# Performance work log

Hardware: AMD Instinct MI355X
Metric: run time of the kernel (lower is better)

## Reference

```python
import jax, jax.numpy as jnp
import numpy as np

K = 9                # snake kernel size
CENTER = K // 2
EXT = 1.0            # extend_scope
EPS = 1e-5           # GroupNorm eps (torch default)


def conv2d(x, w, b, stride, padding):
    out = jax.lax.conv_general_dilated(
        x, w, window_strides=stride, padding=padding,
        dimension_numbers=("NCHW", "OIHW", "NCHW"))
    return out + b[None, :, None, None]


def group_norm(x, gamma, beta, groups):
    B, C, H, W = x.shape
    xg = x.reshape(B, groups, C // groups, H, W)
    mu = xg.mean(axis=(2, 3, 4), keepdims=True)
    var = xg.var(axis=(2, 3, 4), keepdims=True)
    xn = ((xg - mu) / jnp.sqrt(var + EPS)).reshape(B, C, H, W)
    return xn * gamma[None, :, None, None] + beta[None, :, None, None]


def setup_inputs() -> dict:
    key = jax.random.key(0)
    ks = jax.random.split(key, 6)
    B, Cin, Cout, H, W = 4, 64, 64, 128, 128
    x = jax.random.normal(ks[0], (B, Cin, H, W), jnp.float32)
    w_off = jax.random.normal(ks[1], (2 * K, Cin, 3, 3), jnp.float32) * 0.05
    b_off = jax.random.normal(ks[2], (2 * K,), jnp.float32) * 0.01
    g_gn_off = jnp.ones((2 * K,), jnp.float32)
    b_gn_off = jnp.zeros((2 * K,), jnp.float32)
    w_dsc = jax.random.normal(ks[3], (Cout, Cin, K, 1), jnp.float32) * 0.05
    b_dsc = jax.random.normal(ks[4], (Cout,), jnp.float32) * 0.01
    g_gn = jnp.ones((Cout,), jnp.float32)
    b_gn = jnp.zeros((Cout,), jnp.float32)
    return {"x": x, "w_off": w_off, "b_off": b_off,
            "g_gn_off": g_gn_off, "b_gn_off": b_gn_off,
            "w_dsc": w_dsc, "b_dsc": b_dsc, "g_gn": g_gn, "b_gn": b_gn}


def reference(x, w_off, b_off, g_gn_off, b_gn_off, w_dsc, b_dsc, g_gn, b_gn):
    B, Cin, H, W = x.shape
    # offset branch: conv3x3 -> GN(K groups over 2K chans) -> tanh
    off = conv2d(x, w_off, b_off, (1, 1), "SAME")
    off = jnp.tanh(group_norm(off, g_gn_off, b_gn_off, K))
    y_off = off[:, :K]                              # morph=0 uses y offsets, [B,K,H,W]

    # cumulative offsets outward from the kernel center (center entry = 0)
    upper = jnp.cumsum(y_off[:, CENTER + 1:], axis=1)
    lower = jnp.flip(jnp.cumsum(jnp.flip(y_off[:, :CENTER], axis=1), axis=1), axis=1)
    y_off_new = jnp.concatenate(
        [lower, jnp.zeros_like(y_off[:, :1]), upper], axis=1)   # [B,K,H,W]

    # coordinate maps (pixel space)
    y_coord = jnp.arange(H, dtype=x.dtype)[None, None, :, None] + EXT * y_off_new
    x_spread = jnp.linspace(-CENTER, CENTER, K).astype(x.dtype)
    x_coord = jnp.broadcast_to(
        jnp.arange(W, dtype=x.dtype)[None, None, None, :]
        + x_spread[None, :, None, None], y_coord.shape)
    # rearrange b k h w -> b (h k) w
    y_map = y_coord.transpose(0, 2, 1, 3).reshape(B, H * K, W)
    x_map = x_coord.transpose(0, 2, 1, 3).reshape(B, H * K, W)

    # bilinear grid_sample, align_corners=True; clamp-to-range == torch's
    # _coordinate_map_scaling(clamp + [-1,1] normalize) then grid_sample
    yc = jnp.clip(y_map, 0.0, H - 1.0)
    xc = jnp.clip(x_map, 0.0, W - 1.0)
    y0 = jnp.floor(yc); x0 = jnp.floor(xc)
    wy = yc - y0; wx = xc - x0
    y0i = y0.astype(jnp.int32); x0i = x0.astype(jnp.int32)
    y1i = jnp.minimum(y0i + 1, H - 1); x1i = jnp.minimum(x0i + 1, W - 1)

    def samp(f, y0i, y1i, x0i, x1i, wy, wx):
        # f: [C,H,W]; indices/weights: [K*H, W] -> [C, K*H, W]
        v00 = f[:, y0i, x0i]; v01 = f[:, y0i, x1i]
        v10 = f[:, y1i, x0i]; v11 = f[:, y1i, x1i]
        return (v00 * (1 - wy) * (1 - wx) + v01 * (1 - wy) * wx
                + v10 * wy * (1 - wx) + v11 * wy * wx)

    deformed = jax.vmap(samp)(x, y0i, y1i, x0i, x1i, wy, wx)  # [B,C,K*H,W]

    # snake conv: kernel (K,1), stride (K,1), then GN(out//4) + ReLU
    out = conv2d(deformed, w_dsc, b_dsc, (K, 1), "VALID")      # [B,Cout,H,W]
    out = group_norm(out, g_gn, b_gn, w_dsc.shape[0] // 4)
    return jax.nn.relu(out)
```

## Files before the change

kernel.cpp:

```cpp
#include <hip/hip_runtime.h>
#include <hip/hip_bf16.h>
#include <math.h>

#define B 4
#define C 64
#define H 128
#define W 128
#define KK 9
#define CENTER 4
#define HW (H*W)
#define HP 130
#define WP 130

typedef __attribute__((ext_vector_type(8))) short short8;
typedef __attribute__((ext_vector_type(4))) float f4;

#define OFF_OFFT   0
#define OFF_XB     786432
#define OFF_WB     2949632
#define OFF_WOB    2968064
#define OFF_CSUM   2972672
#define OFF_OSUM   2980864

__device__ __forceinline__ unsigned bf16pack(float a, float b) {
    unsigned ua = __builtin_bit_cast(unsigned, a) + 0x8000u;
    unsigned ub = __builtin_bit_cast(unsigned, b) + 0x8000u;
    return __builtin_amdgcn_perm(ub, ua, 0x07060302);
}

__device__ __forceinline__ unsigned lerp_pack(unsigned a, unsigned b, float fw) {
    float alo = __builtin_bit_cast(float, a << 16);
    float ahi = __builtin_bit_cast(float, a & 0xffff0000u);
    float blo = __builtin_bit_cast(float, b << 16);
    float bhi = __builtin_bit_cast(float, b & 0xffff0000u);
    float slo = alo + fw * (blo - alo);
    float shi = ahi + fw * (bhi - ahi);
    return bf16pack(slo, shi);
}

__device__ __forceinline__ float fast_tanh(float x) {
    float e = __expf(2.f * x);
    return 1.f - 2.f * __builtin_amdgcn_rcpf(e + 1.f);
}

__global__ __launch_bounds__(256) void k_prep(const float* __restrict__ x,
                                              const float* __restrict__ w_dsc,
                                              const float* __restrict__ w_off,
                                              unsigned short* __restrict__ xb,
                                              unsigned short* __restrict__ wb,
                                              unsigned short* __restrict__ wob,
                                              float* __restrict__ csum) {
    int bid = blockIdx.x;
    int tid = threadIdx.x;
    if (bid < 2048) {
        __shared__ float lt[64 * 33];
        int xcd = bid & 7, i = bid >> 3;
        int c = i & 3, hc = (i >> 2) & 15, b = i >> 6;
        int h = (xcd << 4) | hc;
        int w0 = c * 32;
        int ciA = tid >> 2, gA = tid & 3;
        int wlB = tid >> 3, cgB = tid & 7;

        if (c == 0 && tid < 8)
            *(uint4*)(xb + ((size_t)(b * HP + h + 1) * WP) * 64 + tid * 8)
                = make_uint4(0, 0, 0, 0);
        if (c == 3 && tid < 8)
            *(uint4*)(xb + (((size_t)(b * HP + h + 1) * WP) + WP - 1) * 64 + tid * 8)
                = make_uint4(0, 0, 0, 0);
        {
            const float* src = x + ((size_t)(b * C + ciA) * HW) + h * W + w0 + gA * 8;
            float4 v0 = *(const float4*)src;
            float4 v1 = *(const float4*)(src + 4);
            float* d = lt + ciA * 33 + gA * 8;
            d[0] = v0.x; d[1] = v0.y; d[2] = v0.z; d[3] = v0.w;
            d[4] = v1.x; d[5] = v1.y; d[6] = v1.z; d[7] = v1.w;
        }
        __syncthreads();
        {
            unsigned u[4];
#pragma unroll
            for (int i2 = 0; i2 < 4; i2++) {
                float lo = lt[(cgB * 8 + 2 * i2)     * 33 + wlB];
                float hi = lt[(cgB * 8 + 2 * i2 + 1) * 33 + wlB];
                u[i2] = bf16pack(lo, hi);
            }
            *(uint4*)(xb + ((size_t)((b * HP + h + 1) * WP + w0 + wlB + 1)) * 64 + cgB * 8) =
                make_uint4(u[0], u[1], u[2], u[3]);
        }
    } else if (bid < 2048 + 8) {
        int r = bid - 2048;
        int b = r >> 1, which = r & 1;
        unsigned short* dst = xb + ((size_t)(b * HP + which * (HP - 1)) * WP) * 64;
        for (int t = tid; t < WP * 64 / 8; t += 256)
            *(uint4*)(dst + t * 8) = make_uint4(0, 0, 0, 0);
    } else if (bid < 2048 + 8 + 180) {
        int idx = (bid - (2048 + 8)) * 256 + tid;
        if (idx < KK * C * C) {
            int k  = idx >> 12;
            int r  = idx & 4095;
            int co = r >> 6;
            int ci = r & 63;
            unsigned u = __builtin_bit_cast(unsigned, w_dsc[(co * C + ci) * KK + k]);
            u = (u + 0x7fffu + ((u >> 16) & 1u)) >> 16;
            wb[idx] = (unsigned short)u;
        } else if (idx < KK * C * C + 9 * 16 * 64) {
            int r   = idx - KK * C * C;
            int tap = r >> 10;
            int j   = (r >> 6) & 15;
            int ci  = r & 63;
            float v = (j < 10) ? w_off[(j * C + ci) * 9 + tap] : 0.f;
            unsigned u = __builtin_bit_cast(unsigned, v);
            u = (u + 0x7fffu + ((u >> 16) & 1u)) >> 16;
            wob[r] = (unsigned short)u;
        }
    } else {
        int z = bid - (2048 + 8 + 180);
        int base = z * 1024 + tid * 4;
        *(f4*)(csum + base) = 0;
    }
}

__global__ __launch_bounds__(256, 4) void k_offconv(const unsigned short* __restrict__ xb,
                                                    const unsigned short* __restrict__ wob,
                                                    const float* __restrict__ b_off,
                                                    float* __restrict__ offT,
                                                    float* __restrict__ osum16) {
    __shared__ unsigned short wlds[1152 * 8];
    __shared__ float red[80];
    int bid = blockIdx.x;
    int xcd  = bid & 7;
    int i    = bid >> 3;
    int b    = i >> 5;
    int rest = i & 31;
    int h    = (xcd << 4) | (rest >> 1);
    int half = rest & 1;
    int tid  = threadIdx.x;
    int wid  = tid >> 6;
    int lane = tid & 63;
    int lm = lane & 15, qd = lane >> 4;
    int pw = half * 64 + wid * 16;

    for (int c = tid; c < 1152; c += 256) {
        int row = c >> 3, g = c & 7;
        uint4 v = *(const uint4*)(wob + c * 8);
        int dst = (g ^ (row & 7)) * 144 + row;
        *(uint4*)(wlds + dst * 8) = v;
    }
    __syncthreads();

    f4 acc = 0;
    const unsigned short* xrow = xb + ((size_t)(b * HP + h) * WP) * 64;
#pragma unroll
    for (int s = 0; s < 2; s++) {
        int co_ofs = s * 32 + qd * 8;
        short8 a_[9];
#pragma unroll
        for (int t = 0; t < 9; t++) {
            int ky = t / 3, kx = t - 3 * (t / 3);
            a_[t] = *(const short8*)(xrow +
                ((size_t)(ky * WP + pw + lm + kx)) * 64 + co_ofs);
        }
#pragma unroll
        for (int t = 0; t < 9; t++) {
            int row = t * 16 + lm;
            int chunk = (((s * 4 + qd) ^ (lm & 7)) * 144) + row;
            short8 w = *(const short8*)(wlds + chunk * 8);
            acc = __builtin_amdgcn_mfma_f32_16x16x32_bf16(a_[t], w, acc, 0, 0, 0);
        }
    }

    float bo = b_off[lm];
    float sv = 0.f, sq = 0.f;
    int pixbase = (b * H + h) * W;
#pragma unroll
    for (int r = 0; r < 4; r++) {
        float val = acc[r] + bo;
        int p = pw + qd * 4 + r;
        if (lm < 10) {
            offT[(size_t)(pixbase + p) * 12 + lm] = val;
            sv += val; sq += val * val;
        }
    }
    sv += __shfl_xor(sv, 16); sv += __shfl_xor(sv, 32);
    sq += __shfl_xor(sq, 16); sq += __shfl_xor(sq, 32);
    if (lane < 16 && lm < 10) {
        red[(wid * 10 + lm) * 2]     = sv;
        red[(wid * 10 + lm) * 2 + 1] = sq;
    }
    __syncthreads();
    if (tid < 20) {
        int j = tid >> 1, comp = tid & 1;
        float s = red[j * 2 + comp] + red[(10 + j) * 2 + comp] +
                  red[(20 + j) * 2 + comp] + red[(30 + j) * 2 + comp];
        int sidx = (h >> 3) & 15;
        atomicAdd(&osum16[sidx * 40 + b * 10 + (j >> 1) * 2 + comp], s);
    }
}

__global__ __launch_bounds__(256, 4) void k_main(const unsigned short* __restrict__ xb,
                                                 const float* __restrict__ offT,
                                                 const float* __restrict__ osum16,
                                                 const float* __restrict__ g_gn_off,
                                                 const float* __restrict__ b_gn_off,
                                                 const unsigned short* __restrict__ wb,
                                                 const float* __restrict__ b_dsc,
                                                 float* __restrict__ outp,
                                                 float* __restrict__ csum16) {
    __shared__ unsigned short wlds[2304 * 8];
    __shared__ float red[512];
    __shared__ float sred[16];

    int bid = blockIdx.x;
    int xcd  = bid & 7;
    int i    = bid >> 3;
    int b    = i >> 5;
    int rest = i & 31;
    int h    = (xcd << 4) | (rest >> 1);
    int p0   = (rest & 1) << 6;
    int tid  = threadIdx.x;
    int wid  = tid >> 6;
    int lane = tid & 63;
    int lm = lane & 15, qd = lane >> 4;

    int ps = p0 + wid * 16 + lm;

    if (tid < 160) {
        int gc = tid >> 4, s = tid & 15;
        float v = osum16[s * 40 + b * 10 + gc];
        v += __shfl_xor(v, 1); v += __shfl_xor(v, 2);
        v += __shfl_xor(v, 4); v += __shfl_xor(v, 8);
        if (s == 0) sred[gc] = v;
    }
    for (int c = tid; c < 2304; c += 256) {
        int k = c >> 8, row = (c >> 2) & 63, g2 = c & 3;
        uint4 v = *(const uint4*)(wb + (size_t)k * 4096 + row * 64 + g2 * 8);
        int dst = ((g2 ^ (row & 3)) * 576) + k * 64 + row;
        *(uint4*)(wlds + dst * 8) = v;
    }
    __syncthreads();

    float yoff[KK];
    {
        const float inv_n = 1.f / (2.f * HW);
        const float* op = offT + (size_t)((b * H + h) * W + ps) * 12;
        f4 o0 = *(const f4*)op;
        f4 o1 = *(const f4*)(op + 4);
        float o8 = op[8];
        float raw[KK] = {o0[0], o0[1], o0[2], o0[3], o1[0], o1[1], o1[2], o1[3], o8};
        float v[KK];
#pragma unroll
        for (int j = 0; j < KK; j++) {
            int g = j >> 1;
            float s  = sred[g * 2];
            float s2 = sred[g * 2 + 1];
            float mean = s * inv_n;
            float var  = s2 * inv_n - mean * mean;
            float rstd = rsqrtf(var + 1e-5f);
            v[j] = fast_tanh((raw[j] - mean) * rstd * g_gn_off[j] + b_gn_off[j]);
        }
        yoff[CENTER] = 0.f;
        float run = 0.f;
#pragma unroll
        for (int k = CENTER - 1; k >= 0; k--) { run += v[k]; yoff[k] = run; }
        run = 0.f;
#pragma unroll
        for (int k = CENTER + 1; k < KK; k++) { run += v[k]; yoff[k] = run; }
    }

    f4 acc[4];
#pragma unroll
    for (int ct = 0; ct < 4; ct++) acc[ct] = 0;

    auto kpass = [&](int s) {
        int so = s * 32;
#pragma unroll
        for (int kg = 0; kg < 3; kg++) {
            int   ofsA[3], ofsB[3];
            float fw[3];
#pragma unroll
            for (int j = 0; j < 3; j++) {
                int k = kg * 3 + j;
                float yc = fminf(fmaxf((float)h + yoff[k], 0.f), (float)(H - 1));
                float fy = floorf(yc);
                int y0 = (int)fy;
                int dy = (y0 < H - 1) ? (WP * 64) : 0;
                fw[j] = yc - fy;
                int xi = min(max(ps + k - CENTER, 0), W - 1);
                ofsA[j] = ((b * HP + y0 + 1) * WP + xi + 1) * 64 + qd * 8 + so;
                ofsB[j] = ofsA[j] + dy;
            }
            uint4 ga[3], gb[3];
#pragma unroll
            for (int j = 0; j < 3; j++) {
                ga[j] = *(const uint4*)(xb + ofsA[j]);
                gb[j] = *(const uint4*)(xb + ofsB[j]);
            }
#pragma unroll
            for (int j = 0; j < 3; j++) {
                int k = kg * 3 + j;
                uint4 r;
                r.x = lerp_pack(ga[j].x, gb[j].x, fw[j]);
                r.y = lerp_pack(ga[j].y, gb[j].y, fw[j]);
                r.z = lerp_pack(ga[j].z, gb[j].z, fw[j]);
                r.w = lerp_pack(ga[j].w, gb[j].w, fw[j]);
                short8 afr = __builtin_bit_cast(short8, r);
#pragma unroll
                for (int ct = 0; ct < 4; ct++) {
                    int row = ct * 16 + lm;
                    int chunk = ((qd ^ (lm & 3)) * 576) + k * 64 + row;
                    short8 bfr = *(const short8*)(wlds + chunk * 8);
                    acc[ct] = __builtin_amdgcn_mfma_f32_16x16x32_bf16(afr, bfr,
                                                                      acc[ct], 0, 0, 0);
                }
            }
        }
    };

    kpass(0);
    __syncthreads();
    for (int c = tid; c < 2304; c += 256) {
        int k = c >> 8, row = (c >> 2) & 63, g2 = c & 3;
        uint4 v = *(const uint4*)(wb + (size_t)k * 4096 + row * 64 + (4 + g2) * 8);
        int dst = ((g2 ^ (row & 3)) * 576) + k * 64 + row;
        *(uint4*)(wlds + dst * 8) = v;
    }
    __syncthreads();
    kpass(1);

#pragma unroll
    for (int ct = 0; ct < 4; ct++) {
        int co = ct * 16 + lm;
        float bias = b_dsc[co];
        f4 v;
        float sv = 0.f, sq = 0.f;
#pragma unroll
        for (int r = 0; r < 4; r++) {
            v[r] = acc[ct][r] + bias;
            sv += v[r]; sq += v[r] * v[r];
        }
        *(f4*)(outp + ((size_t)(b * C + co)) * HW + h * W + p0 + wid * 16 + qd * 4) = v;
        sv += __shfl_xor(sv, 16); sv += __shfl_xor(sv, 32);
        sq += __shfl_xor(sq, 16); sq += __shfl_xor(sq, 32);
        if (lane < 16) {
            red[((wid * 4 + ct) * 16 + lm) * 2]     = sv;
            red[((wid * 4 + ct) * 16 + lm) * 2 + 1] = sq;
        }
    }
    __syncthreads();
    if (tid < 128) {
        int co = tid >> 1, comp = tid & 1;
        int ct = co >> 4, lmr = co & 15;
        float s = 0.f;
#pragma unroll
        for (int w2 = 0; w2 < 4; w2++)
            s += red[((w2 * 4 + ct) * 16 + lmr) * 2 + comp];
        int sidx = (h >> 3) & 15;
        atomicAdd(&csum16[(sidx * 256 + b * 64 + co) * 2 + comp], s);
    }
}

__global__ __launch_bounds__(256) void k_norm(float* __restrict__ outp,
                                              const float* __restrict__ csum16,
                                              const float* __restrict__ g_gn,
                                              const float* __restrict__ b_gn) {
    __shared__ float lds[128];
    int bid = blockIdx.x;
    int xcd = bid & 7;
    int i   = bid >> 3;
    int bc  = i >> 1;
    int c2  = (xcd << 1) | (i & 1);
    int b = bc >> 6, co = bc & 63;
    int grp = co >> 2;
    int tid = threadIdx.x;

    if (tid < 128) {
        int s = tid >> 3, c = (tid >> 1) & 3, comp = tid & 1;
        lds[tid] = csum16[(s * 256 + b * 64 + grp * 4 + c) * 2 + comp];
    }
    __syncthreads();
#pragma unroll
    for (int st = 64; st >= 2; st >>= 1) {
        if (tid < st) lds[tid] += lds[tid + st];
        __syncthreads();
    }
    float S = lds[0], S2 = lds[1];
    float n = 4.f * HW;
    float mean = S / n;
    float var  = S2 / n - mean * mean;
    float rstd = rsqrtf(var + 1e-5f);
    float sc = rstd * g_gn[co];
    float sh = b_gn[co] - mean * sc;

    int idx = (bc * 16 + c2) * 256 + tid;
    float4* ptr = (float4*)outp;
    float4 vv = ptr[idx];
    vv.x = fmaxf(vv.x * sc + sh, 0.f);
    vv.y = fmaxf(vv.y * sc + sh, 0.f);
    vv.z = fmaxf(vv.z * sc + sh, 0.f);
    vv.w = fmaxf(vv.w * sc + sh, 0.f);
    ptr[idx] = vv;
}

extern "C" void kernel_launch(void* const* d_in, const int* in_sizes, int n_in,
                              void* d_out, int out_size, void* d_ws, size_t ws_size,
                              hipStream_t stream) {
    const float* x        = (const float*)d_in[0];
    const float* w_off    = (const float*)d_in[1];
    const float* b_off    = (const float*)d_in[2];
    const float* g_gn_off = (const float*)d_in[3];
    const float* b_gn_off = (const float*)d_in[4];
    const float* w_dsc    = (const float*)d_in[5];
    const float* b_dsc    = (const float*)d_in[6];
    const float* g_gn     = (const float*)d_in[7];
    const float* b_gn     = (const float*)d_in[8];
    float* out = (float*)d_out;
    float* ws  = (float*)d_ws;

    float*          offT   = ws + OFF_OFFT;
    unsigned short* xbp    = (unsigned short*)(ws + OFF_XB);
    unsigned short* wbp    = (unsigned short*)(ws + OFF_WB);
    unsigned short* wobp   = (unsigned short*)(ws + OFF_WOB);
    float*          csum16 = ws + OFF_CSUM;
    float*          osum16 = ws + OFF_OSUM;

    k_prep<<<2048 + 8 + 180 + 9, 256, 0, stream>>>(x, w_dsc, w_off, xbp, wbp,
                                                   wobp, csum16);
    k_offconv<<<2 * B * H, 256, 0, stream>>>(xbp, wobp, b_off, offT, osum16);
    k_main<<<2 * B * H, 256, 0, stream>>>(xbp, offT, osum16, g_gn_off, b_gn_off,
                                          wbp, b_dsc, out, csum16);
    k_norm<<<B * C * HW / 4 / 256, 256, 0, stream>>>(out, csum16, g_gn, b_gn);
}
```

Baseline: 135.5 us.

## Double-buffer weight staging in main kernel, widen prep tiles, simplify norm reduction

After: 142.7 us. +5.3%, slower.

```diff
diff --git a/kernel.cpp b/kernel.cpp
--- a/kernel.cpp
+++ b/kernel.cpp
@@ -52,49 +52,53 @@
                                               float* __restrict__ csum) {
     int bid = blockIdx.x;
     int tid = threadIdx.x;
-    if (bid < 2048) {
-        __shared__ float lt[64 * 33];
+    if (bid < 1024) {
+        __shared__ float lt[64 * 65];
         int xcd = bid & 7, i = bid >> 3;
-        int c = i & 3, hc = (i >> 2) & 15, b = i >> 6;
+        int half = i & 1, hc = (i >> 1) & 15, b = i >> 5;
         int h = (xcd << 4) | hc;
-        int w0 = c * 32;
-        int ciA = tid >> 2, gA = tid & 3;
-        int wlB = tid >> 3, cgB = tid & 7;
-
-        if (c == 0 && tid < 8)
+        int w0 = half * 64;
+
+        if (half == 0 && tid < 8)
             *(uint4*)(xb + ((size_t)(b * HP + h + 1) * WP) * 64 + tid * 8)
                 = make_uint4(0, 0, 0, 0);
-        if (c == 3 && tid < 8)
+        if (half == 1 && tid < 8)
             *(uint4*)(xb + (((size_t)(b * HP + h + 1) * WP) + WP - 1) * 64 + tid * 8)
                 = make_uint4(0, 0, 0, 0);
-        {
-            const float* src = x + ((size_t)(b * C + ciA) * HW) + h * W + w0 + gA * 8;
-            float4 v0 = *(const float4*)src;
-            float4 v1 = *(const float4*)(src + 4);
-            float* d = lt + ciA * 33 + gA * 8;
-            d[0] = v0.x; d[1] = v0.y; d[2] = v0.z; d[3] = v0.w;
-            d[4] = v1.x; d[5] = v1.y; d[6] = v1.z; d[7] = v1.w;
+
+        int ci = tid >> 2, gA = tid & 3;
+        const float* src = x + ((size_t)(b * C + ci) * HW) + h * W + w0 + gA * 16;
+        float4 v[4];
+#pragma unroll
+        for (int j = 0; j < 4; j++) v[j] = *(const float4*)(src + j * 4);
+#pragma unroll
+        for (int j = 0; j < 4; j++) {
+            float* d = lt + ci * 65 + gA * 16 + j * 4;
+            d[0] = v[j].x; d[1] = v[j].y; d[2] = v[j].z; d[3] = v[j].w;
         }
         __syncthreads();
-        {
+#pragma unroll
+        for (int it = 0; it < 2; it++) {
+            int item = tid + it * 256;
+            int px = item >> 3, cg = item & 7;
             unsigned u[4];
 #pragma unroll
             for (int i2 = 0; i2 < 4; i2++) {
-                float lo = lt[(cgB * 8 + 2 * i2)     * 33 + wlB];
-                float hi = lt[(cgB * 8 + 2 * i2 + 1) * 33 + wlB];
+                float lo = lt[(cg * 8 + 2 * i2)     * 65 + px];
+                float hi = lt[(cg * 8 + 2 * i2 + 1) * 65 + px];
                 u[i2] = bf16pack(lo, hi);
             }
-            *(uint4*)(xb + ((size_t)((b * HP + h + 1) * WP + w0 + wlB + 1)) * 64 + cgB * 8) =
-                make_uint4(u[0], u[1], u[2], u[3]);
-        }
-    } else if (bid < 2048 + 8) {
-        int r = bid - 2048;
+            *(uint4*)(xb + ((size_t)((b * HP + h + 1) * WP + w0 + px + 1)) * 64
+                      + cg * 8) = make_uint4(u[0], u[1], u[2], u[3]);
+        }
+    } else if (bid < 1024 + 8) {
+        int r = bid - 1024;
         int b = r >> 1, which = r & 1;
         unsigned short* dst = xb + ((size_t)(b * HP + which * (HP - 1)) * WP) * 64;
         for (int t = tid; t < WP * 64 / 8; t += 256)
             *(uint4*)(dst + t * 8) = make_uint4(0, 0, 0, 0);
-    } else if (bid < 2048 + 8 + 180) {
-        int idx = (bid - (2048 + 8)) * 256 + tid;
+    } else if (bid < 1024 + 8 + 180) {
+        int idx = (bid - (1024 + 8)) * 256 + tid;
         if (idx < KK * C * C) {
             int k  = idx >> 12;
             int r  = idx & 4095;
@@ -114,13 +118,13 @@
             wob[r] = (unsigned short)u;
         }
     } else {
-        int z = bid - (2048 + 8 + 180);
+        int z = bid - (1024 + 8 + 180);
         int base = z * 1024 + tid * 4;
         *(f4*)(csum + base) = 0;
     }
 }
 
-__global__ __launch_bounds__(256, 4) void k_offconv(const unsigned short* __restrict__ xb,
+__global__ __launch_bounds__(256, 8) void k_offconv(const unsigned short* __restrict__ xb,
                                                     const unsigned short* __restrict__ wob,
                                                     const float* __restrict__ b_off,
                                                     float* __restrict__ offT,
@@ -197,7 +201,7 @@
     }
 }
 
-__global__ __launch_bounds__(256, 4) void k_main(const unsigned short* __restrict__ xb,
+__global__ __launch_bounds__(256, 6) void k_main(const unsigned short* __restrict__ xb,
                                                  const float* __restrict__ offT,
                                                  const float* __restrict__ osum16,
                                                  const float* __restrict__ g_gn_off,
@@ -206,9 +210,9 @@
                                                  const float* __restrict__ b_dsc,
                                                  float* __restrict__ outp,
                                                  float* __restrict__ csum16) {
-    __shared__ unsigned short wlds[2304 * 8];
-    __shared__ float red[512];
+    __shared__ unsigned short wlds[2 * 768 * 8];
     __shared__ float sred[16];
+    float* red = (float*)wlds;
 
     int bid = blockIdx.x;
     int xcd  = bid & 7;
@@ -224,6 +228,11 @@
 
     int ps = p0 + wid * 16 + lm;
 
+    const float* op = offT + (size_t)((b * H + h) * W + ps) * 12;
+    f4 o0 = *(const f4*)op;
+    f4 o1 = *(const f4*)(op + 4);
+    float o8 = op[8];
+
     if (tid < 160) {
         int gc = tid >> 4, s = tid & 15;
         float v = osum16[s * 40 + b * 10 + gc];
@@ -231,21 +240,25 @@
         v += __shfl_xor(v, 4); v += __shfl_xor(v, 8);
         if (s == 0) sred[gc] = v;
     }
-    for (int c = tid; c < 2304; c += 256) {
-        int k = c >> 8, row = (c >> 2) & 63, g2 = c & 3;
-        uint4 v = *(const uint4*)(wb + (size_t)k * 4096 + row * 64 + g2 * 8);
-        int dst = ((g2 ^ (row & 3)) * 576) + k * 64 + row;
-        *(uint4*)(wlds + dst * 8) = v;
-    }
+
+    auto stage = [&](int s, int kg, int db) {
+#pragma unroll
+        for (int it = 0; it < 3; it++) {
+            int c = tid + it * 256;
+            int kl = c >> 8, row = (c >> 2) & 63, g2 = c & 3;
+            uint4 v = *(const uint4*)(wb + (size_t)(kg * 3 + kl) * 4096
+                                      + row * 64 + (s * 4 + g2) * 8);
+            int dst = db * 768 + (g2 ^ (row & 3)) * 192 + kl * 64 + row;
+            *(uint4*)(wlds + dst * 8) = v;
+        }
+    };
+
+    stage(0, 0, 0);
     __syncthreads();
 
     float yoff[KK];
     {
         const float inv_n = 1.f / (2.f * HW);
-        const float* op = offT + (size_t)((b * H + h) * W + ps) * 12;
-        f4 o0 = *(const f4*)op;
-        f4 o1 = *(const f4*)(op + 4);
-        float o8 = op[8];
         float raw[KK] = {o0[0], o0[1], o0[2], o0[3], o1[0], o1[1], o1[2], o1[3], o8};
         float v[KK];
 #pragma unroll
@@ -267,65 +280,54 @@
         for (int k = CENTER + 1; k < KK; k++) { run += v[k]; yoff[k] = run; }
     }
 
+    int oA[9], oB[9];
+    float fw9[9];
+#pragma unroll
+    for (int k = 0; k < 9; k++) {
+        float yc = fminf(fmaxf((float)h + yoff[k], 0.f), (float)(H - 1));
+        float fy = floorf(yc);
+        int y0 = (int)fy;
+        int dy = (y0 < H - 1) ? (WP * 64) : 0;
+        fw9[k] = yc - fy;
+        int xi = min(max(ps + k - CENTER, 0), W - 1);
+        oA[k] = ((b * HP + y0 + 1) * WP + xi + 1) * 64 + qd * 8;
+        oB[k] = oA[k] + dy;
+    }
+
     f4 acc[4];
 #pragma unroll
     for (int ct = 0; ct < 4; ct++) acc[ct] = 0;
 
-    auto kpass = [&](int s) {
+    auto consume = [&](int s, int kg, int db) {
         int so = s * 32;
 #pragma unroll
-        for (int kg = 0; kg < 3; kg++) {
-            int   ofsA[3], ofsB[3];
-            float fw[3];
-#pragma unroll
-            for (int j = 0; j < 3; j++) {
-                int k = kg * 3 + j;
-                float yc = fminf(fmaxf((float)h + yoff[k], 0.f), (float)(H - 1));
-                float fy = floorf(yc);
-                int y0 = (int)fy;
-                int dy = (y0 < H - 1) ? (WP * 64) : 0;
-                fw[j] = yc - fy;
-                int xi = min(max(ps + k - CENTER, 0), W - 1);
-                ofsA[j] = ((b * HP + y0 + 1) * WP + xi + 1) * 64 + qd * 8 + so;
-                ofsB[j] = ofsA[j] + dy;
+        for (int kl = 0; kl < 3; kl++) {
+            int k = kg * 3 + kl;
+            uint4 ga = *(const uint4*)(xb + oA[k] + so);
+            uint4 gb = *(const uint4*)(xb + oB[k] + so);
+            uint4 r;
+            r.x = lerp_pack(ga.x, gb.x, fw9[k]);
+            r.y = lerp_pack(ga.y, gb.y, fw9[k]);
+            r.z = lerp_pack(ga.z, gb.z, fw9[k]);
+            r.w = lerp_pack(ga.w, gb.w, fw9[k]);
+            short8 afr = __builtin_bit_cast(short8, r);
+#pragma unroll
+            for (int ct = 0; ct < 4; ct++) {
+                int chunk = db * 768 + ((qd ^ (lm & 3)) * 192) + kl * 64
+                            + ct * 16 + lm;
+                short8 bfr = *(const short8*)(wlds + chunk * 8);
+                acc[ct] = __builtin_amdgcn_mfma_f32_16x16x32_bf16(afr, bfr,
+                                                                  acc[ct], 0, 0, 0);
             }
-            uint4 ga[3], gb[3];
-#pragma unroll
-            for (int j = 0; j < 3; j++) {
-                ga[j] = *(const uint4*)(xb + ofsA[j]);
-                gb[j] = *(const uint4*)(xb + ofsB[j]);
-            }
-#pragma unroll
-            for (int j = 0; j < 3; j++) {
-                int k = kg * 3 + j;
-                uint4 r;
-                r.x = lerp_pack(ga[j].x, gb[j].x, fw[j]);
-                r.y = lerp_pack(ga[j].y, gb[j].y, fw[j]);
-                r.z = lerp_pack(ga[j].z, gb[j].z, fw[j]);
-                r.w = lerp_pack(ga[j].w, gb[j].w, fw[j]);
-                short8 afr = __builtin_bit_cast(short8, r);
-#pragma unroll
-                for (int ct = 0; ct < 4; ct++) {
-                    int row = ct * 16 + lm;
-                    int chunk = ((qd ^ (lm & 3)) * 576) + k * 64 + row;
-                    short8 bfr = *(const short8*)(wlds + chunk * 8);
-                    acc[ct] = __builtin_amdgcn_mfma_f32_16x16x32_bf16(afr, bfr,
-                                                                      acc[ct], 0, 0, 0);
-                }
-            }
         }
     };
 
-    kpass(0);
-    __syncthreads();
-    for (int c = tid; c < 2304; c += 256) {
-        int k = c >> 8, row = (c >> 2) & 63, g2 = c & 3;
-        uint4 v = *(const uint4*)(wb + (size_t)k * 4096 + row * 64 + (4 + g2) * 8);
-        int dst = ((g2 ^ (row & 3)) * 576) + k * 64 + row;
-        *(uint4*)(wlds + dst * 8) = v;
-    }
-    __syncthreads();
-    kpass(1);
+    stage(0, 1, 1); consume(0, 0, 0); __syncthreads();
+    stage(0, 2, 0); consume(0, 1, 1); __syncthreads();
+    stage(1, 0, 1); consume(0, 2, 0); __syncthreads();
+    stage(1, 1, 0); consume(1, 0, 1); __syncthreads();
+    stage(1, 2, 1); consume(1, 1, 0); __syncthreads();
+    consume(1, 2, 1);
 
 #pragma unroll
     for (int ct = 0; ct < 4; ct++) {
@@ -363,42 +365,46 @@
                                               const float* __restrict__ csum16,
                                               const float* __restrict__ g_gn,
                                               const float* __restrict__ b_gn) {
-    __shared__ float lds[128];
+    __shared__ float lds[2];
     int bid = blockIdx.x;
     int xcd = bid & 7;
     int i   = bid >> 3;
-    int bc  = i >> 1;
-    int c2  = (xcd << 1) | (i & 1);
-    int b = bc >> 6, co = bc & 63;
+    int b   = i >> 6, co = i & 63;
     int grp = co >> 2;
     int tid = threadIdx.x;
 
-    if (tid < 128) {
-        int s = tid >> 3, c = (tid >> 1) & 3, comp = tid & 1;
-        lds[tid] = csum16[(s * 256 + b * 64 + grp * 4 + c) * 2 + comp];
+    if (tid < 64) {
+        int s = tid >> 2, c = tid & 3;
+        const float* p = csum16 + (s * 256 + b * 64 + grp * 4 + c) * 2;
+        float v0 = p[0], v1 = p[1];
+#pragma unroll
+        for (int d = 1; d < 64; d <<= 1) {
+            v0 += __shfl_xor(v0, d);
+            v1 += __shfl_xor(v1, d);
+        }
+        if (tid == 0) {
+            float n = 4.f * HW;
+            float mean = v0 / n;
+            float var  = v1 / n - mean * mean;
+            float rstd = rsqrtf(var + 1e-5f);
+            float sc = rstd * g_gn[co];
+            lds[0] = sc;
+            lds[1] = b_gn[co] - mean * sc;
+        }
     }
     __syncthreads();
-#pragma unroll
-    for (int st = 64; st >= 2; st >>= 1) {
-        if (tid < st) lds[tid] += lds[tid + st];
-        __syncthreads();
-    }
-    float S = lds[0], S2 = lds[1];
-    float n = 4.f * HW;
-    float mean = S / n;
-    float var  = S2 / n - mean * mean;
-    float rstd = rsqrtf(var + 1e-5f);
-    float sc = rstd * g_gn[co];
-    float sh = b_gn[co] - mean * sc;
-
-    int idx = (bc * 16 + c2) * 256 + tid;
-    float4* ptr = (float4*)outp;
-    float4 vv = ptr[idx];
-    vv.x = fmaxf(vv.x * sc + sh, 0.f);
-    vv.y = fmaxf(vv.y * sc + sh, 0.f);
-    vv.z = fmaxf(vv.z * sc + sh, 0.f);
-    vv.w = fmaxf(vv.w * sc + sh, 0.f);
-    ptr[idx] = vv;
+    float sc = lds[0], sh = lds[1];
+
+    float4* ptr = (float4*)(outp + ((size_t)(b * C + co)) * HW + xcd * 16 * W);
+#pragma unroll
+    for (int j = 0; j < 2; j++) {
+        float4 vv = ptr[tid + j * 256];
+        vv.x = fmaxf(vv.x * sc + sh, 0.f);
+        vv.y = fmaxf(vv.y * sc + sh, 0.f);
+        vv.z = fmaxf(vv.z * sc + sh, 0.f);
+        vv.w = fmaxf(vv.w * sc + sh, 0.f);
+        ptr[tid + j * 256] = vv;
+    }
 }
 
 extern "C" void kernel_launch(void* const* d_in, const int* in_sizes, int n_in,
@@ -423,10 +429,10 @@
     float*          csum16 = ws + OFF_CSUM;
     float*          osum16 = ws + OFF_OSUM;
 
-    k_prep<<<2048 + 8 + 180 + 9, 256, 0, stream>>>(x, w_dsc, w_off, xbp, wbp,
+    k_prep<<<1024 + 8 + 180 + 9, 256, 0, stream>>>(x, w_dsc, w_off, xbp, wbp,
                                                    wobp, csum16);
     k_offconv<<<2 * B * H, 256, 0, stream>>>(xbp, wobp, b_off, offT, osum16);
     k_main<<<2 * B * H, 256, 0, stream>>>(xbp, offT, osum16, g_gn_off, b_gn_off,
                                           wbp, b_dsc, out, csum16);
-    k_norm<<<B * C * HW / 4 / 256, 256, 0, stream>>>(out, csum16, g_gn, b_gn);
-}
+    k_norm<<<2048, 256, 0, stream>>>(out, csum16, g_gn, b_gn);
+}
```
